# Performance work log

Hardware: AMD Instinct MI355X
Metric: run time of the kernel (lower is better)

## Reference

```python
import jax, jax.numpy as jnp
import numpy as np

N_NODES = 50000
N_EDGES = 800000
NDIM_IN = 64
EDIM = 64
HID = 152  # size_embedding
NDIM_OUT = 64


def _linear(x, W, b):
    # torch nn.Linear: y = x @ W.T + b
    return jnp.matmul(x, W.T) + b


def _sage_layer(nf, ef, Wm, bm, Wa, ba, src, dst):
    # message: gather src node feats, concat edge feats, linear -> [E,1,F]
    m = _linear(jnp.concatenate([nf[src], ef], axis=2), Wm, bm)
    # mean scatter-reduce to dst nodes (zero for nodes with no in-edges)
    s = jax.ops.segment_sum(m, dst, num_segments=N_NODES)
    deg = jax.ops.segment_sum(jnp.ones((m.shape[0],), m.dtype), dst, num_segments=N_NODES)
    h_neigh = s / jnp.maximum(deg, 1.0)[:, None, None]
    # update: concat self + neighbor agg, linear, relu
    return jax.nn.relu(_linear(jnp.concatenate([nf, h_neigh], axis=2), Wa, ba))


def setup_inputs() -> dict:
    key = jax.random.key(0)
    ks = jax.random.split(key, 16)
    def lin_params(kw, kb, fan_in, fan_out):
        bound = 1.0 / np.sqrt(fan_in)
        W = jax.random.uniform(kw, (fan_out, fan_in), jnp.float32, -bound, bound)
        b = jax.random.uniform(kb, (fan_out,), jnp.float32, -bound, bound)
        return W, b
    nfeats = jax.random.normal(ks[0], (N_NODES, 1, NDIM_IN), jnp.float32)
    efeats = jax.random.normal(ks[1], (N_EDGES, 1, EDIM), jnp.float32)
    src = jax.random.randint(ks[2], (N_EDGES,), 0, N_NODES, jnp.int32)
    dst = jax.random.randint(ks[3], (N_EDGES,), 0, N_NODES, jnp.int32)
    Wm1, bm1 = lin_params(ks[4], ks[5], NDIM_IN + EDIM, HID)
    Wa1, ba1 = lin_params(ks[6], ks[7], NDIM_IN + HID, HID)
    Wm2, bm2 = lin_params(ks[8], ks[9], HID + EDIM, HID)
    Wa2, ba2 = lin_params(ks[10], ks[11], HID + HID, HID)
    Wm3, bm3 = lin_params(ks[12], ks[13], HID + EDIM, NDIM_OUT)
    Wa3, ba3 = lin_params(ks[14], ks[15], HID + NDIM_OUT, NDIM_OUT)
    return {
        "nfeats": nfeats, "efeats": efeats,
        "Wm1": Wm1, "bm1": bm1, "Wa1": Wa1, "ba1": ba1,
        "Wm2": Wm2, "bm2": bm2, "Wa2": Wa2, "ba2": ba2,
        "Wm3": Wm3, "bm3": bm3, "Wa3": Wa3, "ba3": ba3,
        "src": src, "dst": dst,
    }


def reference(nfeats, efeats, Wm1, bm1, Wa1, ba1, Wm2, bm2, Wa2, ba2,
              Wm3, bm3, Wa3, ba3, src, dst):
    # dropout is identity in eval mode
    h = _sage_layer(nfeats, efeats, Wm1, bm1, Wa1, ba1, src, dst)
    h = _sage_layer(h, efeats, Wm2, bm2, Wa2, ba2, src, dst)
    h = _sage_layer(h, efeats, Wm3, bm3, Wa3, ba3, src, dst)
    return h.sum(axis=1)  # [N, ndim_out]
```

## Files before the change

kernel.cpp:

```cpp
#include <hip/hip_runtime.h>


#define NN 50000
#define NE 800000
#define NIN 64
#define EDIM_ 64
#define HID_ 152
#define NOUT 64
#define PADN 50176

__global__ __launch_bounds__(256) void hist_kernel(const int* __restrict__ dst,
                                                   int* __restrict__ ideg) {
    int e = blockIdx.x * 256 + threadIdx.x;
    if (e < NE) atomicAdd(&ideg[dst[e]], 1);
}

__global__ __launch_bounds__(256) void scan1_kernel(const int* __restrict__ in,
                                                    int* __restrict__ out,
                                                    int* __restrict__ bsum) {
    __shared__ int ws[4];
    int t = threadIdx.x;
    int base = blockIdx.x * 1024 + t * 4;
    int a0 = in[base], a1 = in[base + 1], a2 = in[base + 2], a3 = in[base + 3];
    int s = a0 + a1 + a2 + a3;
    int lane = t & 63, wid = t >> 6;
    int v = s;
#pragma unroll
    for (int d = 1; d < 64; d <<= 1) {
        int u = __shfl_up(v, d);
        if (lane >= d) v += u;
    }
    if (lane == 63) ws[wid] = v;
    __syncthreads();
    int wofs = 0;
    if (wid > 0) wofs += ws[0];
    if (wid > 1) wofs += ws[1];
    if (wid > 2) wofs += ws[2];
    int excl = wofs + v - s;
    out[base] = excl;
    out[base + 1] = excl + a0;
    out[base + 2] = excl + a0 + a1;
    out[base + 3] = excl + a0 + a1 + a2;
    if (t == 255) bsum[blockIdx.x] = wofs + v;
}

__global__ __launch_bounds__(64) void scan2_kernel(int* __restrict__ bsum, int nb) {
    int t = threadIdx.x;
    int orig = (t < nb) ? bsum[t] : 0;
    int v = orig;
#pragma unroll
    for (int d = 1; d < 64; d <<= 1) {
        int u = __shfl_up(v, d);
        if (t >= d) v += u;
    }
    if (t < nb) bsum[t] = v - orig;
}

__global__ __launch_bounds__(256) void scan3_kernel(int* __restrict__ out,
                                                    const int* __restrict__ bsum) {
    int base = blockIdx.x * 1024 + threadIdx.x * 4;
    int b = bsum[blockIdx.x];
    out[base] += b; out[base + 1] += b; out[base + 2] += b; out[base + 3] += b;
}

__global__ __launch_bounds__(256) void scatter_edges_kernel(const int* __restrict__ src,
                                                            const int* __restrict__ dst,
                                                            int* __restrict__ cursor,
                                                            int* __restrict__ csr_nf,
                                                            int* __restrict__ csr_ef) {
    int e = blockIdx.x * 256 + threadIdx.x;
    if (e >= NE) return;
    int d = dst[e];
    int pos = atomicAdd(&cursor[d], 1);
    csr_nf[pos] = src[e];
    csr_ef[pos] = e;
}

template <int F>
__global__ __launch_bounds__(256) void agg_kernel(const float* __restrict__ table,
                                                  const int* __restrict__ rows,
                                                  const int* __restrict__ off,
                                                  float* __restrict__ out) {
    constexpr int C = F / 4;
    constexpr int NPW = 64 / C;
    int t = threadIdx.x;
    int lane = t & 63, wid = t >> 6;
    int sub = lane / C;
    int ch = lane - sub * C;
    int n = (blockIdx.x * 4 + wid) * NPW + sub;
    if (sub >= NPW || n >= NN) return;
    int s = off[n], e = off[n + 1];
    float ax0 = 0.f, ax1 = 0.f, ax2 = 0.f, ax3 = 0.f;
    float bx0 = 0.f, bx1 = 0.f, bx2 = 0.f, bx3 = 0.f;
    int i = s;
    for (; i + 1 < e; i += 2) {
        int r0 = rows[i], r1 = rows[i + 1];
        float4 v0 = *(const float4*)(table + (size_t)r0 * F + ch * 4);
        float4 v1 = *(const float4*)(table + (size_t)r1 * F + ch * 4);
        ax0 += v0.x; ax1 += v0.y; ax2 += v0.z; ax3 += v0.w;
        bx0 += v1.x; bx1 += v1.y; bx2 += v1.z; bx3 += v1.w;
    }
    if (i < e) {
        int r0 = rows[i];
        float4 v0 = *(const float4*)(table + (size_t)r0 * F + ch * 4);
        ax0 += v0.x; ax1 += v0.y; ax2 += v0.z; ax3 += v0.w;
    }
    float4 r;
    r.x = ax0 + bx0; r.y = ax1 + bx1; r.z = ax2 + bx2; r.w = ax3 + bx3;
    *(float4*)(out + (size_t)n * F + ch * 4) = r;
}

template <int K1, int K2, int NT, bool MSG>
__global__ __launch_bounds__(256) void gemm_kernel(const float* __restrict__ X1,
                                                   const float* __restrict__ X2,
                                                   const float* __restrict__ W,
                                                   const float* __restrict__ bias,
                                                   const int* __restrict__ off,
                                                   float* __restrict__ out) {
    constexpr int KT = K1 + K2;
    __shared__ float Xs[8][68];
    __shared__ float Ws[8][68];
    const int t = threadIdx.x;
    const int m0 = blockIdx.x * 64;
    const int n0 = blockIdx.y * 64;
    const int lm = t >> 2;
    const int lk = (t & 3) * 2;
    const int tx = t & 15;
    const int ty = t >> 4;
    float acc[4][4] = {};

    const bool xrow_ok = (m0 + lm) < NN;
    const bool wrow_ok = (n0 + lm) < NT;

#pragma unroll
    for (int seg = 0; seg < 2; ++seg) {
        const float* __restrict__ X = seg ? X2 : X1;
        const int K = seg ? K2 : K1;
        const int koff = seg ? K1 : 0;
        for (int k0 = 0; k0 < K; k0 += 8) {
            float2 xv = make_float2(0.f, 0.f);
            if (xrow_ok) xv = *(const float2*)(X + (size_t)(m0 + lm) * K + k0 + lk);
            float2 wv = make_float2(0.f, 0.f);
            if (wrow_ok) wv = *(const float2*)(W + (size_t)(n0 + lm) * KT + koff + k0 + lk);
            __syncthreads();
            Xs[lk][lm] = xv.x; Xs[lk + 1][lm] = xv.y;
            Ws[lk][lm] = wv.x; Ws[lk + 1][lm] = wv.y;
            __syncthreads();
#pragma unroll
            for (int k = 0; k < 8; ++k) {
                float a0 = Xs[k][ty * 4 + 0], a1 = Xs[k][ty * 4 + 1];
                float a2 = Xs[k][ty * 4 + 2], a3 = Xs[k][ty * 4 + 3];
                float b0 = Ws[k][tx * 4 + 0], b1 = Ws[k][tx * 4 + 1];
                float b2 = Ws[k][tx * 4 + 2], b3 = Ws[k][tx * 4 + 3];
                acc[0][0] += a0 * b0; acc[0][1] += a0 * b1; acc[0][2] += a0 * b2; acc[0][3] += a0 * b3;
                acc[1][0] += a1 * b0; acc[1][1] += a1 * b1; acc[1][2] += a1 * b2; acc[1][3] += a1 * b3;
                acc[2][0] += a2 * b0; acc[2][1] += a2 * b1; acc[2][2] += a2 * b2; acc[2][3] += a2 * b3;
                acc[3][0] += a3 * b0; acc[3][1] += a3 * b1; acc[3][2] += a3 * b2; acc[3][3] += a3 * b3;
            }
        }
    }

    const int o0 = n0 + tx * 4;
    if (o0 >= NT) return;
    float b0 = bias[o0], b1 = bias[o0 + 1], b2 = bias[o0 + 2], b3 = bias[o0 + 3];
#pragma unroll
    for (int i = 0; i < 4; ++i) {
        int n = m0 + ty * 4 + i;
        if (n >= NN) break;
        float4 r;
        if (MSG) {
            float d = (float)(off[n + 1] - off[n]);
            float inv = 1.0f / fmaxf(d, 1.0f);
            r.x = (acc[i][0] + d * b0) * inv;
            r.y = (acc[i][1] + d * b1) * inv;
            r.z = (acc[i][2] + d * b2) * inv;
            r.w = (acc[i][3] + d * b3) * inv;
        } else {
            r.x = fmaxf(acc[i][0] + b0, 0.0f);
            r.y = fmaxf(acc[i][1] + b1, 0.0f);
            r.z = fmaxf(acc[i][2] + b2, 0.0f);
            r.w = fmaxf(acc[i][3] + b3, 0.0f);
        }
        *(float4*)(out + (size_t)n * NT + o0) = r;
    }
}

extern "C" void kernel_launch(void* const* d_in, const int* in_sizes, int n_in,
                              void* d_out, int out_size, void* d_ws, size_t ws_size,
                              hipStream_t stream) {
    const float* nfeats = (const float*)d_in[0];
    const float* efeats = (const float*)d_in[1];
    const float* Wm1 = (const float*)d_in[2];
    const float* bm1 = (const float*)d_in[3];
    const float* Wa1 = (const float*)d_in[4];
    const float* ba1 = (const float*)d_in[5];
    const float* Wm2 = (const float*)d_in[6];
    const float* bm2 = (const float*)d_in[7];
    const float* Wa2 = (const float*)d_in[8];
    const float* ba2 = (const float*)d_in[9];
    const float* Wm3 = (const float*)d_in[10];
    const float* bm3 = (const float*)d_in[11];
    const float* Wa3 = (const float*)d_in[12];
    const float* ba3 = (const float*)d_in[13];
    const int* src = (const int*)d_in[14];
    const int* dst = (const int*)d_in[15];
    float* out = (float*)d_out;

    int* iws = (int*)d_ws;
    int* ideg   = iws;
    int* off    = iws + PADN;
    int* cursor = iws + 2 * PADN;
    int* csr_nf = iws + 3 * PADN;
    int* csr_ef = csr_nf + NE;
    float* B = (float*)(csr_ef + NE);
    float* P = B + 3200000;
    float* Q = P + 7600000;
    float* R = Q + 7600000;

    const int BLK = 256;
    auto cdiv = [](long long a, long long b) { return (int)((a + b - 1) / b); };
    dim3 g152(cdiv(NN, 64), cdiv(152, 64));
    dim3 g64(cdiv(NN, 64), 1);
    const int NB = PADN / 1024;

    hipMemsetAsync(ideg, 0, (size_t)PADN * 4, stream);
    hist_kernel<<<cdiv(NE, BLK), BLK, 0, stream>>>(dst, ideg);
    scan1_kernel<<<NB, 256, 0, stream>>>(ideg, off, cursor);
    scan2_kernel<<<1, 64, 0, stream>>>(cursor, NB);
    scan3_kernel<<<NB, 256, 0, stream>>>(off, cursor);
    hipMemcpyAsync(cursor, off, (size_t)NN * 4, hipMemcpyDeviceToDevice, stream);
    scatter_edges_kernel<<<cdiv(NE, BLK), BLK, 0, stream>>>(src, dst, cursor, csr_nf, csr_ef);

    agg_kernel<EDIM_><<<cdiv(NN, 16), BLK, 0, stream>>>(efeats, csr_ef, off, B);

    agg_kernel<NIN><<<cdiv(NN, 16), BLK, 0, stream>>>(nfeats, csr_nf, off, P);
    gemm_kernel<NIN, EDIM_, HID_, true><<<g152, BLK, 0, stream>>>(P, B, Wm1, bm1, off, Q);
    gemm_kernel<NIN, HID_, HID_, false><<<g152, BLK, 0, stream>>>(nfeats, Q, Wa1, ba1, off, R);

    agg_kernel<HID_><<<cdiv(NN, 4), BLK, 0, stream>>>(R, csr_nf, off, P);
    gemm_kernel<HID_, EDIM_, HID_, true><<<g152, BLK, 0, stream>>>(P, B, Wm2, bm2, off, Q);
    gemm_kernel<HID_, HID_, HID_, false><<<g152, BLK, 0, stream>>>(R, Q, Wa2, ba2, off, P);

    agg_kernel<HID_><<<cdiv(NN, 4), BLK, 0, stream>>>(P, csr_nf, off, Q);
    gemm_kernel<HID_, EDIM_, NOUT, true><<<g64, BLK, 0, stream>>>(Q, B, Wm3, bm3, off, R);
    gemm_kernel<HID_, NOUT, NOUT, false><<<g64, BLK, 0, stream>>>(P, R, Wa3, ba3, off, out);
}
```

Before: 912.5 us.

## Widen per-lane gather vectors and enlarge GEMM register tile to 8x4

The aggregation kernel now has each lane accumulate 8 floats instead of 4, packing more nodes per wavefront and raising lane utilisation for the 152-wide features. The GEMM kernel switches from a 64x64 to a 128x64 block tile, with each thread computing an 8x4 output using float4 shared-memory reads. This aims to raise arithmetic per shared-memory load and the number of gathers in flight. In exchange there are fewer GEMM blocks and more registers per thread, which may reduce occupancy.

```diff
diff --git a/kernel.cpp b/kernel.cpp
--- a/kernel.cpp
+++ b/kernel.cpp
@@ -81,7 +81,7 @@
                                                   const int* __restrict__ rows,
                                                   const int* __restrict__ off,
                                                   float* __restrict__ out) {
-    constexpr int C = F / 4;
+    constexpr int C = F / 8;
     constexpr int NPW = 64 / C;
     int t = threadIdx.x;
     int lane = t & 63, wid = t >> 6;
@@ -90,24 +90,33 @@
     int n = (blockIdx.x * 4 + wid) * NPW + sub;
     if (sub >= NPW || n >= NN) return;
     int s = off[n], e = off[n + 1];
-    float ax0 = 0.f, ax1 = 0.f, ax2 = 0.f, ax3 = 0.f;
-    float bx0 = 0.f, bx1 = 0.f, bx2 = 0.f, bx3 = 0.f;
+    float4 a0 = {0,0,0,0}, a1 = {0,0,0,0}, b0 = {0,0,0,0}, b1 = {0,0,0,0};
     int i = s;
     for (; i + 1 < e; i += 2) {
-        int r0 = rows[i], r1 = rows[i + 1];
-        float4 v0 = *(const float4*)(table + (size_t)r0 * F + ch * 4);
-        float4 v1 = *(const float4*)(table + (size_t)r1 * F + ch * 4);
-        ax0 += v0.x; ax1 += v0.y; ax2 += v0.z; ax3 += v0.w;
-        bx0 += v1.x; bx1 += v1.y; bx2 += v1.z; bx3 += v1.w;
+        const float* p0 = table + (size_t)rows[i] * F + ch * 8;
+        const float* p1 = table + (size_t)rows[i + 1] * F + ch * 8;
+        float4 u0 = *(const float4*)p0;
+        float4 u1 = *(const float4*)(p0 + 4);
+        float4 v0 = *(const float4*)p1;
+        float4 v1 = *(const float4*)(p1 + 4);
+        a0.x += u0.x; a0.y += u0.y; a0.z += u0.z; a0.w += u0.w;
+        a1.x += u1.x; a1.y += u1.y; a1.z += u1.z; a1.w += u1.w;
+        b0.x += v0.x; b0.y += v0.y; b0.z += v0.z; b0.w += v0.w;
+        b1.x += v1.x; b1.y += v1.y; b1.z += v1.z; b1.w += v1.w;
     }
     if (i < e) {
-        int r0 = rows[i];
-        float4 v0 = *(const float4*)(table + (size_t)r0 * F + ch * 4);
-        ax0 += v0.x; ax1 += v0.y; ax2 += v0.z; ax3 += v0.w;
-    }
-    float4 r;
-    r.x = ax0 + bx0; r.y = ax1 + bx1; r.z = ax2 + bx2; r.w = ax3 + bx3;
-    *(float4*)(out + (size_t)n * F + ch * 4) = r;
+        const float* p0 = table + (size_t)rows[i] * F + ch * 8;
+        float4 u0 = *(const float4*)p0;
+        float4 u1 = *(const float4*)(p0 + 4);
+        a0.x += u0.x; a0.y += u0.y; a0.z += u0.z; a0.w += u0.w;
+        a1.x += u1.x; a1.y += u1.y; a1.z += u1.z; a1.w += u1.w;
+    }
+    float4 r0, r1;
+    r0.x = a0.x + b0.x; r0.y = a0.y + b0.y; r0.z = a0.z + b0.z; r0.w = a0.w + b0.w;
+    r1.x = a1.x + b1.x; r1.y = a1.y + b1.y; r1.z = a1.z + b1.z; r1.w = a1.w + b1.w;
+    float* o = out + (size_t)n * F + ch * 8;
+    *(float4*)o = r0;
+    *(float4*)(o + 4) = r1;
 }
 
 template <int K1, int K2, int NT, bool MSG>
@@ -118,19 +127,21 @@
                                                    const int* __restrict__ off,
                                                    float* __restrict__ out) {
     constexpr int KT = K1 + K2;
-    __shared__ float Xs[8][68];
+    __shared__ float Xs[8][132];
     __shared__ float Ws[8][68];
     const int t = threadIdx.x;
-    const int m0 = blockIdx.x * 64;
+    const int m0 = blockIdx.x * 128;
     const int n0 = blockIdx.y * 64;
-    const int lm = t >> 2;
-    const int lk = (t & 3) * 2;
+    const int xrow = t >> 1;
+    const int xk = (t & 1) * 4;
+    const int wrow = t >> 2;
+    const int wk = (t & 3) * 2;
     const int tx = t & 15;
     const int ty = t >> 4;
-    float acc[4][4] = {};
-
-    const bool xrow_ok = (m0 + lm) < NN;
-    const bool wrow_ok = (n0 + lm) < NT;
+    float acc[8][4] = {};
+
+    const bool xrow_ok = (m0 + xrow) < NN;
+    const bool wrow_ok = (n0 + wrow) < NT;
 
 #pragma unroll
     for (int seg = 0; seg < 2; ++seg) {
@@ -138,24 +149,28 @@
         const int K = seg ? K2 : K1;
         const int koff = seg ? K1 : 0;
         for (int k0 = 0; k0 < K; k0 += 8) {
-            float2 xv = make_float2(0.f, 0.f);
-            if (xrow_ok) xv = *(const float2*)(X + (size_t)(m0 + lm) * K + k0 + lk);
+            float4 xv = make_float4(0.f, 0.f, 0.f, 0.f);
+            if (xrow_ok) xv = *(const float4*)(X + (size_t)(m0 + xrow) * K + k0 + xk);
             float2 wv = make_float2(0.f, 0.f);
-            if (wrow_ok) wv = *(const float2*)(W + (size_t)(n0 + lm) * KT + koff + k0 + lk);
+            if (wrow_ok) wv = *(const float2*)(W + (size_t)(n0 + wrow) * KT + koff + k0 + wk);
             __syncthreads();
-            Xs[lk][lm] = xv.x; Xs[lk + 1][lm] = xv.y;
-            Ws[lk][lm] = wv.x; Ws[lk + 1][lm] = wv.y;
+            Xs[xk][xrow] = xv.x; Xs[xk + 1][xrow] = xv.y;
+            Xs[xk + 2][xrow] = xv.z; Xs[xk + 3][xrow] = xv.w;
+            Ws[wk][wrow] = wv.x; Ws[wk + 1][wrow] = wv.y;
             __syncthreads();
 #pragma unroll
             for (int k = 0; k < 8; ++k) {
-                float a0 = Xs[k][ty * 4 + 0], a1 = Xs[k][ty * 4 + 1];
-                float a2 = Xs[k][ty * 4 + 2], a3 = Xs[k][ty * 4 + 3];
-                float b0 = Ws[k][tx * 4 + 0], b1 = Ws[k][tx * 4 + 1];
-                float b2 = Ws[k][tx * 4 + 2], b3 = Ws[k][tx * 4 + 3];
-                acc[0][0] += a0 * b0; acc[0][1] += a0 * b1; acc[0][2] += a0 * b2; acc[0][3] += a0 * b3;
-                acc[1][0] += a1 * b0; acc[1][1] += a1 * b1; acc[1][2] += a1 * b2; acc[1][3] += a1 * b3;
-                acc[2][0] += a2 * b0; acc[2][1] += a2 * b1; acc[2][2] += a2 * b2; acc[2][3] += a2 * b3;
-                acc[3][0] += a3 * b0; acc[3][1] += a3 * b1; acc[3][2] += a3 * b2; acc[3][3] += a3 * b3;
+                float4 a0 = *(const float4*)&Xs[k][ty * 8];
+                float4 a1 = *(const float4*)&Xs[k][ty * 8 + 4];
+                float4 b = *(const float4*)&Ws[k][tx * 4];
+                acc[0][0] += a0.x * b.x; acc[0][1] += a0.x * b.y; acc[0][2] += a0.x * b.z; acc[0][3] += a0.x * b.w;
+                acc[1][0] += a0.y * b.x; acc[1][1] += a0.y * b.y; acc[1][2] += a0.y * b.z; acc[1][3] += a0.y * b.w;
+                acc[2][0] += a0.z * b.x; acc[2][1] += a0.z * b.y; acc[2][2] += a0.z * b.z; acc[2][3] += a0.z * b.w;
+                acc[3][0] += a0.w * b.x; acc[3][1] += a0.w * b.y; acc[3][2] += a0.w * b.z; acc[3][3] += a0.w * b.w;
+                acc[4][0] += a1.x * b.x; acc[4][1] += a1.x * b.y; acc[4][2] += a1.x * b.z; acc[4][3] += a1.x * b.w;
+                acc[5][0] += a1.y * b.x; acc[5][1] += a1.y * b.y; acc[5][2] += a1.y * b.z; acc[5][3] += a1.y * b.w;
+                acc[6][0] += a1.z * b.x; acc[6][1] += a1.z * b.y; acc[6][2] += a1.z * b.z; acc[6][3] += a1.z * b.w;
+                acc[7][0] += a1.w * b.x; acc[7][1] += a1.w * b.y; acc[7][2] += a1.w * b.z; acc[7][3] += a1.w * b.w;
             }
         }
     }
@@ -164,8 +179,8 @@
     if (o0 >= NT) return;
     float b0 = bias[o0], b1 = bias[o0 + 1], b2 = bias[o0 + 2], b3 = bias[o0 + 3];
 #pragma unroll
-    for (int i = 0; i < 4; ++i) {
-        int n = m0 + ty * 4 + i;
+    for (int i = 0; i < 8; ++i) {
+        int n = m0 + ty * 8 + i;
         if (n >= NN) break;
         float4 r;
         if (MSG) {
@@ -219,8 +234,8 @@
 
     const int BLK = 256;
     auto cdiv = [](long long a, long long b) { return (int)((a + b - 1) / b); };
-    dim3 g152(cdiv(NN, 64), cdiv(152, 64));
-    dim3 g64(cdiv(NN, 64), 1);
+    dim3 g152(cdiv(NN, 128), cdiv(152, 64));
+    dim3 g64(cdiv(NN, 128), 1);
     const int NB = PADN / 1024;
 
     hipMemsetAsync(ideg, 0, (size_t)PADN * 4, stream);
@@ -231,17 +246,17 @@
     hipMemcpyAsync(cursor, off, (size_t)NN * 4, hipMemcpyDeviceToDevice, stream);
     scatter_edges_kernel<<<cdiv(NE, BLK), BLK, 0, stream>>>(src, dst, cursor, csr_nf, csr_ef);
 
-    agg_kernel<EDIM_><<<cdiv(NN, 16), BLK, 0, stream>>>(efeats, csr_ef, off, B);
-
-    agg_kernel<NIN><<<cdiv(NN, 16), BLK, 0, stream>>>(nfeats, csr_nf, off, P);
+    agg_kernel<EDIM_><<<cdiv(NN, 32), BLK, 0, stream>>>(efeats, csr_ef, off, B);
+
+    agg_kernel<NIN><<<cdiv(NN, 32), BLK, 0, stream>>>(nfeats, csr_nf, off, P);
     gemm_kernel<NIN, EDIM_, HID_, true><<<g152, BLK, 0, stream>>>(P, B, Wm1, bm1, off, Q);
     gemm_kernel<NIN, HID_, HID_, false><<<g152, BLK, 0, stream>>>(nfeats, Q, Wa1, ba1, off, R);
 
-    agg_kernel<HID_><<<cdiv(NN, 4), BLK, 0, stream>>>(R, csr_nf, off, P);
+    agg_kernel<HID_><<<cdiv(NN, 12), BLK, 0, stream>>>(R, csr_nf, off, P);
     gemm_kernel<HID_, EDIM_, HID_, true><<<g152, BLK, 0, stream>>>(P, B, Wm2, bm2, off, Q);
     gemm_kernel<HID_, HID_, HID_, false><<<g152, BLK, 0, stream>>>(R, Q, Wa2, ba2, off, P);
 
-    agg_kernel<HID_><<<cdiv(NN, 4), BLK, 0, stream>>>(P, csr_nf, off, Q);
+    agg_kernel<HID_><<<cdiv(NN, 12), BLK, 0, stream>>>(P, csr_nf, off, Q);
     gemm_kernel<HID_, EDIM_, NOUT, true><<<g64, BLK, 0, stream>>>(Q, B, Wm3, bm3, off, R);
     gemm_kernel<HID_, NOUT, NOUT, false><<<g64, BLK, 0, stream>>>(P, R, Wa3, ba3, off, out);
 }
```

After: 923.6 us. No clear change (+1.2%).
